# Kernel tuning notes

Measured on AMD Instinct MI355X. Metric: run time of the kernel, lower is better.

## Reference

```python
import jax, jax.numpy as jnp
import numpy as np

B, NQ, D, H, L, P, FFN = 32, 300, 256, 8, 3, 4, 1024
SPATIAL = [(80, 80), (40, 40), (20, 20)]  # static multi-scale feature shapes (640px, strides 8/16/32)
S = sum(h * w for h, w in SPATIAL)  # 8400
HD = D // H


def _ln(x, g, b, eps=1e-5):
    m = jnp.mean(x, -1, keepdims=True)
    v = jnp.mean((x - m) ** 2, -1, keepdims=True)
    return (x - m) * jax.lax.rsqrt(v + eps) * g + b


def _grid_sample(img, grid):
    # img: (N,C,Hh,Ww); grid: (N,Q,Pp,2) in [-1,1]; bilinear, zeros padding, align_corners=False
    N, C, Hh, Ww = img.shape
    x = (grid[..., 0] + 1.0) * (Ww * 0.5) - 0.5
    y = (grid[..., 1] + 1.0) * (Hh * 0.5) - 0.5
    x0 = jnp.floor(x)
    y0 = jnp.floor(y)
    wx1 = x - x0
    wy1 = y - y0
    x0i = x0.astype(jnp.int32)
    y0i = y0.astype(jnp.int32)
    flat = img.reshape(N, C, Hh * Ww)
    Q, Pp = grid.shape[1], grid.shape[2]

    def corner(xi, yi, w):
        valid = (xi >= 0) & (xi < Ww) & (yi >= 0) & (yi < Hh)
        idx = jnp.clip(yi, 0, Hh - 1) * Ww + jnp.clip(xi, 0, Ww - 1)
        v = jnp.take_along_axis(flat, idx.reshape(N, 1, Q * Pp), axis=2).reshape(N, C, Q, Pp)
        return v * (w * valid)[:, None]

    return (corner(x0i, y0i, (1 - wx1) * (1 - wy1))
            + corner(x0i + 1, y0i, wx1 * (1 - wy1))
            + corner(x0i, y0i + 1, (1 - wx1) * wy1)
            + corner(x0i + 1, y0i + 1, wx1 * wy1))


def setup_inputs() -> dict:
    key = jax.random.key(0)
    ks = iter(jax.random.split(key, 32))
    inp = {
        'hidden_states': jax.random.normal(next(ks), (B, NQ, D), jnp.float32),
        'position_embeddings': jax.random.normal(next(ks), (B, NQ, D), jnp.float32),
        'reference_points': jax.random.uniform(next(ks), (B, NQ, 1, 4), jnp.float32, 0.1, 0.9),
        'encoder_hidden_states': jax.random.normal(next(ks), (B, S, D), jnp.float32),
    }
    for name, shape in [('Wq', (D, D)), ('Wk', (D, D)), ('Wv', (D, D)), ('Wo', (D, D)),
                        ('Woff', (D, H * L * P * 2)), ('Waw', (D, H * L * P)),
                        ('Wval', (D, D)), ('Wout', (D, D)), ('W1', (D, FFN)), ('W2', (FFN, D))]:
        inp[name] = jax.random.normal(next(ks), shape, jnp.float32) * 0.02
    for name, dim in [('bq', D), ('bk', D), ('bv', D), ('bo', D), ('boff', H * L * P * 2),
                      ('baw', H * L * P), ('bval', D), ('bout', D), ('b1', FFN), ('b2', D)]:
        inp[name] = jnp.zeros((dim,), jnp.float32)
    for g, bname in [('ln1_g', 'ln1_b'), ('ln2_g', 'ln2_b'), ('ln3_g', 'ln3_b')]:
        inp[g] = jnp.ones((D,), jnp.float32)
        inp[bname] = jnp.zeros((D,), jnp.float32)
    return inp


def reference(hidden_states, position_embeddings, reference_points, encoder_hidden_states,
              Wq, bq, Wk, bk, Wv, bv, Wo, bo, ln1_g, ln1_b,
              Woff, boff, Waw, baw, Wval, bval, Wout, bout, ln2_g, ln2_b,
              W1, b1, W2, b2, ln3_g, ln3_b):
    hs = hidden_states
    # ---- self attention (pos-embedded q/k, raw v) ----
    hp = hs + position_embeddings
    q = ((hp @ Wq + bq) * (HD ** -0.5)).reshape(B, NQ, H, HD)
    k = (hp @ Wk + bk).reshape(B, NQ, H, HD)
    v = (hs @ Wv + bv).reshape(B, NQ, H, HD)
    attn = jax.nn.softmax(jnp.einsum('bqhd,bkhd->bhqk', q, k), axis=-1)
    sa = jnp.einsum('bhqk,bkhd->bqhd', attn, v).reshape(B, NQ, D) @ Wo + bo
    hs = _ln(hs + sa, ln1_g, ln1_b)
    # ---- multi-scale deformable cross attention ----
    hp = hs + position_embeddings
    value = (encoder_hidden_states @ Wval + bval).reshape(B, S, H, HD)
    off = (hp @ Woff + boff).reshape(B, NQ, H, L, P, 2)
    aw = jax.nn.softmax((hp @ Waw + baw).reshape(B, NQ, H, L * P), axis=-1).reshape(B, NQ, H, L, P)
    ref = reference_points  # (B,NQ,1,4) boxes -> 4-coord branch
    loc = ref[:, :, None, :, None, :2] + off / P * ref[:, :, None, :, None, 2:] * 0.5
    grids = (2.0 * loc - 1.0).transpose(0, 2, 1, 3, 4, 5).reshape(B * H, NQ, L, P, 2)
    start = 0
    samples = []
    for lvl, (hh, ww) in enumerate(SPATIAL):
        v_l = value[:, start:start + hh * ww]  # (B,hw,H,HD)
        start += hh * ww
        v_l = v_l.transpose(0, 2, 3, 1).reshape(B * H, HD, hh, ww)
        samples.append(_grid_sample(v_l, grids[:, :, lvl]))  # (B*H,HD,NQ,P)
    sampled = jnp.stack(samples, axis=3).reshape(B * H, HD, NQ, L * P)
    w = aw.transpose(0, 2, 1, 3, 4).reshape(B * H, 1, NQ, L * P)
    ca = (sampled * w).sum(-1).reshape(B, H * HD, NQ).transpose(0, 2, 1) @ Wout + bout
    hs = _ln(hs + ca, ln2_g, ln2_b)
    # ---- FFN ----
    ff = jax.nn.relu(hs @ W1 + b1) @ W2 + b2
    return _ln(hs + ff, ln3_g, ln3_b)
```

## Files before the change

kernel.cpp:

```cpp
#include <hip/hip_runtime.h>
#include <hip/hip_bf16.h>

typedef unsigned int  uint32;
typedef unsigned short ushort16;
typedef __bf16 bfx8 __attribute__((ext_vector_type(8)));
typedef float  f32x4 __attribute__((ext_vector_type(4)));

typedef __attribute__((address_space(1))) const unsigned int gas_u32;
typedef __attribute__((address_space(3))) unsigned int las_u32;

#define B_   32
#define NQ_  300
#define D_   256
#define H_   8
#define HD_  32
#define L_   3
#define P_   4
#define S_   8400
#define FFN_ 1024
#define M1   (B_*NQ_)
#define MV   (B_*S_)
#define NQP  320
#define NQT  19

__device__ inline ushort16 f2bf(float x) {
  uint32 u = __float_as_uint(x);
  uint32 r = u + 0x7fffu + ((u >> 16) & 1u);
  return (ushort16)(r >> 16);
}
__device__ inline uint32 cvtpk(float lo, float hi) {
  uint32 r; asm("v_cvt_pk_bf16_f32 %0, %1, %2" : "=v"(r) : "v"(lo), "v"(hi)); return r;
}

struct WPrep {
  const float* src[9];
  ushort16*    dst[9];
  int K[9], N[9], Npad[9], tileEnd[9];
  float scale[9];
  const float* wval; ushort16* wvalc;
  const float* bqs;  const float* bks;  float* bqk;
  const float* boffs; const float* baws; float* boffaw;
};

__global__ __launch_bounds__(256) void rt_wprep(WPrep a)
{
  __shared__ float t[32][33];
  int blk = blockIdx.x;
  if (blk < 904) {
    int wi = 0;
    while (blk >= a.tileEnd[wi]) wi++;
    int base = wi ? a.tileEnd[wi - 1] : 0;
    int idx = blk - base;
    int K = a.K[wi], N = a.N[wi];
    int ntx = a.Npad[wi] / 32;
    int n0 = (idx % ntx) * 32, k0 = (idx / ntx) * 32;
    float sc = a.scale[wi];
    const float* W = a.src[wi];
    ushort16* WT = a.dst[wi];
    int c = threadIdx.x & 31, r = threadIdx.x >> 5;
#pragma unroll
    for (int i = 0; i < 4; i++) {
      int nn = n0 + c;
      t[r + i * 8][c] = (nn < N) ? W[(size_t)(k0 + r + i * 8) * N + nn] : 0.f;
    }
    __syncthreads();
#pragma unroll
    for (int i = 0; i < 4; i++)
      WT[(size_t)(n0 + r + i * 8) * K + k0 + c] = f2bf(t[c][r + i * 8] * sc);
  } else if (blk < 936) {
    int gid = (blk - 904) * 256 + threadIdx.x;
    int c = gid >> 8, n = gid & 255;
    const float* W = a.wval;
    uint4 u;
    u.x = (uint32)f2bf(W[(c*8+0)*256 + n]) | ((uint32)f2bf(W[(c*8+1)*256 + n]) << 16);
    u.y = (uint32)f2bf(W[(c*8+2)*256 + n]) | ((uint32)f2bf(W[(c*8+3)*256 + n]) << 16);
    u.z = (uint32)f2bf(W[(c*8+4)*256 + n]) | ((uint32)f2bf(W[(c*8+5)*256 + n]) << 16);
    u.w = (uint32)f2bf(W[(c*8+6)*256 + n]) | ((uint32)f2bf(W[(c*8+7)*256 + n]) << 16);
    *(uint4*)&a.wvalc[(size_t)c * 2048 + n * 8] = u;
  } else if (blk == 936) {
    a.bqk[threadIdx.x] = a.bqs[threadIdx.x] * a.scale[0];
  } else if (blk == 937) {
    a.bqk[256 + threadIdx.x] = a.bks[threadIdx.x];
  } else if (blk == 938) {
    if (threadIdx.x < 192) a.boffaw[threadIdx.x] = a.boffs[threadIdx.x];
  } else {
    if (threadIdx.x < 96) a.boffaw[192 + threadIdx.x] = a.baws[threadIdx.x];
  }
}

__global__ __launch_bounds__(1024, 1) void rt_vgemm(
    const float* __restrict__ A, const ushort16* __restrict__ BC,
    const float* __restrict__ bias, ushort16* __restrict__ Vout)
{
  __shared__ __align__(16) char ldsB[131072];
  const int tid = threadIdx.x;
  const int lane = tid & 63, w = tid >> 6;
  const int l15 = lane & 15, l4 = lane >> 4;

#pragma unroll
  for (int i = 0; i < 8; ++i)
    __builtin_amdgcn_global_load_lds(
        (gas_u32*)(const void*)((const char*)BC + tid * 16 + i * 16384),
        (las_u32*)(void*)(&ldsB[tid * 16 + i * 16384]), 16, 0, 0);
  __syncthreads();

  const int wrow = w * 16 + l15;
  for (int t = blockIdx.x; t < MV / 256; t += 256) {
    const float* Ap = A + ((size_t)t * 256 + wrow) * 256 + l4 * 8;
    f32x4 aA = *(const f32x4*)(Ap);
    f32x4 aB = *(const f32x4*)(Ap + 4);
    f32x4 aC = *(const f32x4*)(Ap + 32);
    f32x4 aD = *(const f32x4*)(Ap + 36);
    f32x4 acc[16];
#pragma unroll
    for (int i = 0; i < 16; ++i) acc[i] = (f32x4){0.f, 0.f, 0.f, 0.f};

#pragma unroll
    for (int tt = 0; tt < 4; ++tt) {
      {
        uint4 u;
        u.x = cvtpk(aA[0], aA[1]); u.y = cvtpk(aA[2], aA[3]);
        u.z = cvtpk(aB[0], aB[1]); u.w = cvtpk(aB[2], aB[3]);
        bfx8 af = __builtin_bit_cast(bfx8, u);
        if (tt < 3) {
          aA = *(const f32x4*)(Ap + (2 * tt + 2) * 32);
          aB = *(const f32x4*)(Ap + (2 * tt + 2) * 32 + 4);
        }
        const char* bp = &ldsB[(2 * tt * 4 + l4) * 4096 + l15 * 16];
#pragma unroll
        for (int ni = 0; ni < 16; ++ni) {
          bfx8 bg = *(const bfx8*)(const void*)(bp + ni * 256);
          acc[ni] = __builtin_amdgcn_mfma_f32_16x16x32_bf16(bg, af, acc[ni], 0, 0, 0);
        }
      }
      {
        uint4 u;
        u.x = cvtpk(aC[0], aC[1]); u.y = cvtpk(aC[2], aC[3]);
        u.z = cvtpk(aD[0], aD[1]); u.w = cvtpk(aD[2], aD[3]);
        bfx8 af = __builtin_bit_cast(bfx8, u);
        if (tt < 3) {
          aC = *(const f32x4*)(Ap + (2 * tt + 3) * 32);
          aD = *(const f32x4*)(Ap + (2 * tt + 3) * 32 + 4);
        }
        const char* bp = &ldsB[((2 * tt + 1) * 4 + l4) * 4096 + l15 * 16];
#pragma unroll
        for (int ni = 0; ni < 16; ++ni) {
          bfx8 bg = *(const bfx8*)(const void*)(bp + ni * 256);
          acc[ni] = __builtin_amdgcn_mfma_f32_16x16x32_bf16(bg, af, acc[ni], 0, 0, 0);
        }
      }
    }
    int row = t * 256 + wrow;
    int bb = row / S_, s = row - bb * S_;
    ushort16* vb = Vout + (((size_t)bb * H_) * S_ + s) * HD_;
#pragma unroll
    for (int ni = 0; ni < 16; ++ni) {
      int col = ni * 16 + l4 * 4;
      f32x4 bv = *(const f32x4*)(bias + col);
      int hh = col >> 5, hd = col & 31;
      uint2 st;
      st.x = cvtpk(acc[ni][0] + bv[0], acc[ni][1] + bv[1]);
      st.y = cvtpk(acc[ni][2] + bv[2], acc[ni][3] + bv[3]);
      *(uint2*)(vb + (size_t)hh * S_ * HD_ + hd) = st;
    }
  }
}

#define GBM 128
#define GBN 128
#define GBK 32
#define LDP 40

__global__ __launch_bounds__(256) void rt_mgemm(
    const float* __restrict__ A, const float* __restrict__ A2,
    const ushort16* __restrict__ BT, const float* __restrict__ bias,
    float* __restrict__ C,
    ushort16* __restrict__ Sc, ushort16* __restrict__ Sc2,
    int M, int N, int K, float scale, int mode)
{
  __shared__ __align__(16) ushort16 As[GBM][LDP];
  __shared__ __align__(16) ushort16 Bs[GBN][LDP];
  const int tid  = threadIdx.x;
  const int lane = tid & 63;
  const int w    = tid >> 6;
  const int wr   = (w >> 1) * 64;
  const int wc   = (w & 1) * 64;
  const int bm   = blockIdx.y * GBM;
  const int bn   = blockIdx.x * GBN;
  const int l15  = lane & 15;
  const int l4   = lane >> 4;

  f32x4 acc[4][4];
#pragma unroll
  for (int i = 0; i < 4; i++)
#pragma unroll
    for (int j = 0; j < 4; j++)
      acc[i][j] = (f32x4){0.f, 0.f, 0.f, 0.f};

  const int arow = tid >> 3, akc = tid & 7;
  const int brow = tid >> 2, bkc = tid & 3;

  for (int k0 = 0; k0 < K; k0 += GBK) {
#pragma unroll
    for (int i = 0; i < 4; i++) {
      int row = arow + i * 32;
      f32x4 v = *(const f32x4*)(A + (size_t)(bm + row) * K + k0 + akc * 4);
      if (A2) {
        f32x4 v2 = *(const f32x4*)(A2 + (size_t)(bm + row) * K + k0 + akc * 4);
#pragma unroll
        for (int r = 0; r < 4; r++) v[r] += v2[r];
      }
      uint2 u;
      u.x = cvtpk(v.x, v.y);
      u.y = cvtpk(v.z, v.w);
      *(uint2*)(&As[row][akc * 4]) = u;
    }
#pragma unroll
    for (int i = 0; i < 2; i++) {
      int row = brow + i * 64;
      uint4 v = *(const uint4*)(BT + (size_t)(bn + row) * K + k0 + bkc * 8);
      *(uint4*)(&Bs[row][bkc * 8]) = v;
    }
    __syncthreads();

    bfx8 af[4], bg[4];
#pragma unroll
    for (int mi = 0; mi < 4; mi++)
      af[mi] = *(const bfx8*)(&As[wr + mi * 16 + l15][l4 * 8]);
#pragma unroll
    for (int ni = 0; ni < 4; ni++)
      bg[ni] = *(const bfx8*)(&Bs[wc + ni * 16 + l15][l4 * 8]);
#pragma unroll
    for (int mi = 0; mi < 4; mi++)
#pragma unroll
      for (int ni = 0; ni < 4; ni++)
        acc[mi][ni] = __builtin_amdgcn_mfma_f32_16x16x32_bf16(af[mi], bg[ni], acc[mi][ni], 0, 0, 0);
    __syncthreads();
  }

#pragma unroll
  for (int mi = 0; mi < 4; mi++) {
#pragma unroll
    for (int ni = 0; ni < 4; ni++) {
      int col = bn + wc + ni * 16 + l15;
      if (col >= N) continue;
      float bv = bias[col];
#pragma unroll
      for (int r = 0; r < 4; r++) {
        int row = bm + wr + mi * 16 + l4 * 4 + r;
        float vv = (acc[mi][ni][r] + bv) * scale;
        if (mode == 1) vv = fmaxf(vv, 0.f);
        if (mode == 3) {
          int bb = row / NQ_, q = row - bb * NQ_;
          int hh = col >> 5, hd = col & 31;
          Sc[(((size_t)bb * H_ + hh) * NQP + q) * HD_ + hd] = f2bf(vv);
        } else if (mode == 4) {
          int bb = row / NQ_, q = row - bb * NQ_;
          int hh = col >> 5, hd = col & 31;
          ushort16* d = (hh < 8) ? Sc : Sc2;
          d[(((size_t)bb * H_ + (hh & 7)) * NQP + q) * HD_ + hd] = f2bf(vv);
        } else {
          C[(size_t)row * N + col] = vv;
        }
      }
    }
  }
}

__global__ __launch_bounds__(256) void rt_vtr(const ushort16* __restrict__ vh,
                                              ushort16* __restrict__ vt)
{
  __shared__ ushort16 t[64][33];
  int bh = blockIdx.x;
  const ushort16* src = vh + (size_t)bh * NQP * HD_;
  ushort16* dst = vt + (size_t)bh * HD_ * NQP;
  int tid = threadIdx.x;
  int lrow = tid >> 2, lc8 = (tid & 3) * 8;
  int ohd = tid >> 3, oq8 = (tid & 7) * 8;
  for (int r0 = 0; r0 < NQP; r0 += 64) {
    uint4 v = {0u, 0u, 0u, 0u};
    if (r0 + lrow < NQ_)
      v = *(const uint4*)(src + (size_t)(r0 + lrow) * HD_ + lc8);
    ushort16* tp = &t[lrow][lc8];
    tp[0] = (ushort16)(v.x & 0xffff); tp[1] = (ushort16)(v.x >> 16);
    tp[2] = (ushort16)(v.y & 0xffff); tp[3] = (ushort16)(v.y >> 16);
    tp[4] = (ushort16)(v.z & 0xffff); tp[5] = (ushort16)(v.z >> 16);
    tp[6] = (ushort16)(v.w & 0xffff); tp[7] = (ushort16)(v.w >> 16);
    __syncthreads();
    uint4 o;
    o.x = (uint32)t[oq8 + 0][ohd] | ((uint32)t[oq8 + 1][ohd] << 16);
    o.y = (uint32)t[oq8 + 2][ohd] | ((uint32)t[oq8 + 3][ohd] << 16);
    o.z = (uint32)t[oq8 + 4][ohd] | ((uint32)t[oq8 + 5][ohd] << 16);
    o.w = (uint32)t[oq8 + 6][ohd] | ((uint32)t[oq8 + 7][ohd] << 16);
    *(uint4*)(dst + (size_t)ohd * NQP + r0 + oq8) = o;
    __syncthreads();
  }
}

__global__ __launch_bounds__(256) void rt_fattn(
    const ushort16* __restrict__ qh, const ushort16* __restrict__ kh,
    const ushort16* __restrict__ vt, float* __restrict__ O)
{
  int gw  = blockIdx.x * 4 + (threadIdx.x >> 6);
  int bh  = gw / NQT, qt = gw - bh * NQT;
  int b   = bh >> 3, h = bh & 7;
  int lane = threadIdx.x & 63;
  int l15 = lane & 15, l4 = lane >> 4;
  int kb4 = l4 * 4;
  const ushort16* Qb = qh + (size_t)bh * NQP * HD_;
  const ushort16* Kb = kh + (size_t)bh * NQP * HD_;
  const ushort16* Vb = vt + (size_t)bh * HD_ * NQP;
  int q = qt * 16 + l15;

  bfx8 bgQ = *(const bfx8*)(const void*)(Qb + (size_t)q * HD_ + l4 * 8);
  f32x4 o0 = {0.f,0.f,0.f,0.f}, o1 = {0.f,0.f,0.f,0.f};
  float m = -1e30f, ssum = 0.f;

  for (int k0 = 0; k0 < NQP; k0 += 32) {
    bfx8 afk0 = *(const bfx8*)(const void*)(Kb + (size_t)(k0 + l15) * HD_ + l4 * 8);
    bfx8 afk1 = *(const bfx8*)(const void*)(Kb + (size_t)(k0 + 16 + l15) * HD_ + l4 * 8);
    f32x4 z = {0.f,0.f,0.f,0.f};
    f32x4 s0 = __builtin_amdgcn_mfma_f32_16x16x32_bf16(afk0, bgQ, z, 0, 0, 0);
    f32x4 s1 = __builtin_amdgcn_mfma_f32_16x16x32_bf16(afk1, bgQ, z, 0, 0, 0);
    int ka = k0 + kb4, kbb = k0 + 16 + kb4;
#pragma unroll
    for (int r = 0; r < 4; r++) {
      if (ka  + r >= NQ_) s0[r] = -1e30f;
      if (kbb + r >= NQ_) s1[r] = -1e30f;
    }
    float cm = fmaxf(fmaxf(fmaxf(s0[0], s0[1]), fmaxf(s0[2], s0[3])),
                     fmaxf(fmaxf(s1[0], s1[1]), fmaxf(s1[2], s1[3])));
    cm = fmaxf(cm, __shfl_xor(cm, 16));
    cm = fmaxf(cm, __shfl_xor(cm, 32));
    float nm = fmaxf(m, cm);
    float sc = __expf(m - nm);
    m = nm;
    f32x4 p0, p1;
#pragma unroll
    for (int r = 0; r < 4; r++) { p0[r] = __expf(s0[r] - m); p1[r] = __expf(s1[r] - m); }
    float ls = (p0[0]+p0[1]+p0[2]+p0[3]) + (p1[0]+p1[1]+p1[2]+p1[3]);
    ls += __shfl_xor(ls, 16);
    ls += __shfl_xor(ls, 32);
    ssum = ssum * sc + ls;

    uint32 t0w0 = cvtpk(p0[0], p0[1]);
    uint32 t0w1 = cvtpk(p0[2], p0[3]);
    uint32 t1w0 = cvtpk(p1[0], p1[1]);
    uint32 t1w1 = cvtpk(p1[2], p1[3]);
    int srcA = l15 + 32 * (l4 & 1);
    int srcB = srcA + 16;
    uint32 a00 = __shfl((int)t0w0, srcA), a01 = __shfl((int)t0w1, srcA);
    uint32 b00 = __shfl((int)t0w0, srcB), b01 = __shfl((int)t0w1, srcB);
    uint32 a10 = __shfl((int)t1w0, srcA), a11 = __shfl((int)t1w1, srcA);
    uint32 b10 = __shfl((int)t1w0, srcB), b11 = __shfl((int)t1w1, srcB);
    bool hi = (l4 >= 2);
    uint4 pw;
    pw.x = hi ? a10 : a00;
    pw.y = hi ? a11 : a01;
    pw.z = hi ? b10 : b00;
    pw.w = hi ? b11 : b01;
    bfx8 bgP = __builtin_bit_cast(bfx8, pw);

    bfx8 afv0 = *(const bfx8*)(const void*)(Vb + (size_t)l15 * NQP + k0 + l4 * 8);
    bfx8 afv1 = *(const bfx8*)(const void*)(Vb + (size_t)(16 + l15) * NQP + k0 + l4 * 8);
#pragma unroll
    for (int r = 0; r < 4; r++) { o0[r] *= sc; o1[r] *= sc; }
    o0 = __builtin_amdgcn_mfma_f32_16x16x32_bf16(afv0, bgP, o0, 0, 0, 0);
    o1 = __builtin_amdgcn_mfma_f32_16x16x32_bf16(afv1, bgP, o1, 0, 0, 0);
  }

  if (q < NQ_) {
    float inv = 1.f / ssum;
    float* op = O + ((size_t)(b * NQ_ + q)) * D_ + h * HD_ + kb4;
    f32x4 r0, r1;
#pragma unroll
    for (int r = 0; r < 4; r++) { r0[r] = o0[r] * inv; r1[r] = o1[r] * inv; }
    *(f32x4*)op = r0;
    *(f32x4*)(op + 16) = r1;
  }
}

__global__ __launch_bounds__(256) void rt_ln2(
    const float* __restrict__ X, const float* __restrict__ R1,
    const float* __restrict__ R2,
    const float* __restrict__ g, const float* __restrict__ be,
    float* __restrict__ O, int rows)
{
  int row = blockIdx.x * 4 + (threadIdx.x >> 6);
  int lane = threadIdx.x & 63;
  if (row >= rows) return;
  size_t base = (size_t)row * D_ + lane * 4;
  float4 x = *(const float4*)(X + base);
  float4 r = *(const float4*)(R1 + base);
  float v0 = x.x + r.x, v1 = x.y + r.y, v2 = x.z + r.z, v3 = x.w + r.w;
  if (R2) {
    float4 r2 = *(const float4*)(R2 + base);
    v0 += r2.x; v1 += r2.y; v2 += r2.z; v3 += r2.w;
  }
  float s = v0 + v1 + v2 + v3;
  float sq = v0*v0 + v1*v1 + v2*v2 + v3*v3;
#pragma unroll
  for (int o = 32; o >= 1; o >>= 1) { s += __shfl_xor(s, o); sq += __shfl_xor(sq, o); }
  float mean = s * (1.f / D_);
  float var  = sq * (1.f / D_) - mean * mean;
  float inv  = 1.f / sqrtf(var + 1e-5f);
  int c = lane * 4;
  float4 gv = *(const float4*)(g + c);
  float4 bv = *(const float4*)(be + c);
  float4 o4;
  o4.x = (v0 - mean) * inv * gv.x + bv.x;
  o4.y = (v1 - mean) * inv * gv.y + bv.y;
  o4.z = (v2 - mean) * inv * gv.z + bv.z;
  o4.w = (v3 - mean) * inv * gv.w + bv.w;
  *(float4*)(O + base) = o4;
}

__device__ inline void rt_acc8(const ushort16* p, float wgt, float* acc) {
  uint4 v = *(const uint4*)(const void*)p;
  acc[0] += wgt * __uint_as_float(v.x << 16);
  acc[1] += wgt * __uint_as_float(v.x & 0xffff0000u);
  acc[2] += wgt * __uint_as_float(v.y << 16);
  acc[3] += wgt * __uint_as_float(v.y & 0xffff0000u);
  acc[4] += wgt * __uint_as_float(v.z << 16);
  acc[5] += wgt * __uint_as_float(v.z & 0xffff0000u);
  acc[6] += wgt * __uint_as_float(v.w << 16);
  acc[7] += wgt * __uint_as_float(v.w & 0xffff0000u);
}

__global__ __launch_bounds__(256) void rt_deform(
    const ushort16* __restrict__ value,
    const float* __restrict__ offaw,
    const float* __restrict__ ref,
    float* __restrict__ O)
{
  int gid = blockIdx.x * 256 + threadIdx.x;
  int hd0 = (gid & 3) * 8;
  int bqh = gid >> 2;
  int h   = bqh & 7;
  int bq  = bqh >> 3;
  int b   = bq / NQ_;
  const float* rp = ref + (size_t)bq * 4;
  float rx = rp[0], ry = rp[1];
  float rw = rp[2] * 0.125f, rh = rp[3] * 0.125f;
  const float* op = offaw + (size_t)bq * 288 + h * 24;
  const float* ap = offaw + (size_t)bq * 288 + 192 + h * 12;
  float e[12]; float mx = -1e30f;
#pragma unroll
  for (int i = 0; i < 12; i++) { e[i] = ap[i]; mx = fmaxf(mx, e[i]); }
  float ssum = 0.f;
#pragma unroll
  for (int i = 0; i < 12; i++) { e[i] = __expf(e[i] - mx); ssum += e[i]; }
  float sinv = 1.f / ssum;

  const ushort16* vb = value + ((size_t)b * H_ + h) * (size_t)S_ * HD_ + hd0;
  float acc[8];
#pragma unroll
  for (int i = 0; i < 8; i++) acc[i] = 0.f;
  const int starts[3] = {0, 6400, 8000};
  const int dims[3]   = {80, 40, 20};
#pragma unroll
  for (int l = 0; l < L_; l++) {
    const int Wl = dims[l];
    const ushort16* vl = vb + (size_t)starts[l] * HD_;
#pragma unroll
    for (int p = 0; p < P_; p++) {
      int ip = l * P_ + p;
      float wgt = e[ip] * sinv;
      float x = (rx + op[ip*2+0] * rw) * Wl - 0.5f;
      float y = (ry + op[ip*2+1] * rh) * Wl - 0.5f;
      float x0f = floorf(x), y0f = floorf(y);
      int   x0 = (int)x0f,  y0 = (int)y0f;
      float wx1 = x - x0f, wy1 = y - y0f;
      float wx0 = 1.f - wx1, wy0 = 1.f - wy1;
      bool xok0 = (x0 >= 0) & (x0 < Wl), xok1 = (x0+1 >= 0) & (x0+1 < Wl);
      bool yok0 = (y0 >= 0) & (y0 < Wl), yok1 = (y0+1 >= 0) & (y0+1 < Wl);
      const ushort16* r0p = vl + (size_t)(y0 * Wl) * HD_;
      const ushort16* r1p = r0p + (size_t)Wl * HD_;
      if (xok0 & yok0) rt_acc8(r0p + (size_t)x0 * HD_,     wgt * wx0 * wy0, acc);
      if (xok1 & yok0) rt_acc8(r0p + (size_t)(x0+1) * HD_, wgt * wx1 * wy0, acc);
      if (xok0 & yok1) rt_acc8(r1p + (size_t)x0 * HD_,     wgt * wx0 * wy1, acc);
      if (xok1 & yok1) rt_acc8(r1p + (size_t)(x0+1) * HD_, wgt * wx1 * wy1, acc);
    }
  }
  float* outp = O + (size_t)bq * D_ + h * HD_ + hd0;
  float4 a0, a1;
  a0.x = acc[0]; a0.y = acc[1]; a0.z = acc[2]; a0.w = acc[3];
  a1.x = acc[4]; a1.y = acc[5]; a1.z = acc[6]; a1.w = acc[7];
  *(float4*)outp = a0;
  *(float4*)(outp + 4) = a1;
}

extern "C" void kernel_launch(void* const* d_in, const int* in_sizes, int n_in,
                              void* d_out, int out_size, void* d_ws, size_t ws_size,
                              hipStream_t stream)
{
  const float* hs   = (const float*)d_in[0];
  const float* pos  = (const float*)d_in[1];
  const float* ref  = (const float*)d_in[2];
  const float* ehs  = (const float*)d_in[3];
  const float* Wq   = (const float*)d_in[4];
  const float* Wk   = (const float*)d_in[5];
  const float* Wv   = (const float*)d_in[6];
  const float* Wo   = (const float*)d_in[7];
  const float* Woff = (const float*)d_in[8];
  const float* Waw  = (const float*)d_in[9];
  const float* Wval = (const float*)d_in[10];
  const float* Wout = (const float*)d_in[11];
  const float* W1   = (const float*)d_in[12];
  const float* W2   = (const float*)d_in[13];
  const float* bq   = (const float*)d_in[14];
  const float* bk   = (const float*)d_in[15];
  const float* bvv  = (const float*)d_in[16];
  const float* bo   = (const float*)d_in[17];
  const float* boff = (const float*)d_in[18];
  const float* baw  = (const float*)d_in[19];
  const float* bval = (const float*)d_in[20];
  const float* bout = (const float*)d_in[21];
  const float* b1   = (const float*)d_in[22];
  const float* b2   = (const float*)d_in[23];
  const float* ln1g = (const float*)d_in[24];
  const float* ln1b = (const float*)d_in[25];
  const float* ln2g = (const float*)d_in[26];
  const float* ln2b = (const float*)d_in[27];
  const float* ln3g = (const float*)d_in[28];
  const float* ln3b = (const float*)d_in[29];
  float* out = (float*)d_out;

  float* ws = (float*)d_ws;
  ushort16* value = (ushort16*)ws;
  float* t0     = ws + 36864000;
  float* t1     = ws + 39321600;
  float* hs1    = ws + 41779200;
  float* hs2    = ws + 44236800;
  float* offawb = ws + 46694400;
  float* ffn1   = ws + 49459200;
  ushort16* qh = (ushort16*)(ws + 59289600);
  ushort16* kh = (ushort16*)(ws + 60600320);
  ushort16* vh = (ushort16*)(ws + 61911040);
  ushort16* vt = (ushort16*)(ws + 63221760);
  ushort16* wbase  = (ushort16*)(ws + 64532480);
  ushort16* WqkT   = wbase;
  ushort16* WvT    = WqkT   + 131072;
  ushort16* WoT    = WvT    + 65536;
  ushort16* WoffawT= WoT    + 65536;
  ushort16* WoutT  = WoffawT+ 98304;
  ushort16* W1T    = WoutT  + 65536;
  ushort16* W2T    = W1T    + 262144;
  ushort16* WvalC  = W2T    + 262144;
  float* bqk    = (float*)(WvalC + 65536);
  float* boffaw = bqk + 512;

  const float qscale = 0.17677669529663687f;

  WPrep a;
  a.src[0]=Wq;   a.dst[0]=WqkT;            a.K[0]=256;  a.N[0]=256;  a.Npad[0]=256; a.scale[0]=qscale;
  a.src[1]=Wk;   a.dst[1]=WqkT+65536;      a.K[1]=256;  a.N[1]=256;  a.Npad[1]=256; a.scale[1]=1.f;
  a.src[2]=Wv;   a.dst[2]=WvT;             a.K[2]=256;  a.N[2]=256;  a.Npad[2]=256; a.scale[2]=1.f;
  a.src[3]=Wo;   a.dst[3]=WoT;             a.K[3]=256;  a.N[3]=256;  a.Npad[3]=256; a.scale[3]=1.f;
  a.src[4]=Woff; a.dst[4]=WoffawT;         a.K[4]=256;  a.N[4]=192;  a.Npad[4]=192; a.scale[4]=1.f;
  a.src[5]=Waw;  a.dst[5]=WoffawT+49152;   a.K[5]=256;  a.N[5]=96;   a.Npad[5]=96;  a.scale[5]=1.f;
  a.src[6]=Wout; a.dst[6]=WoutT;           a.K[6]=256;  a.N[6]=256;  a.Npad[6]=256; a.scale[6]=1.f;
  a.src[7]=W1;   a.dst[7]=W1T;             a.K[7]=256;  a.N[7]=1024; a.Npad[7]=1024;a.scale[7]=1.f;
  a.src[8]=W2;   a.dst[8]=W2T;             a.K[8]=1024; a.N[8]=256;  a.Npad[8]=256; a.scale[8]=1.f;
  int cum = 0;
  int tiles[9] = {64, 64, 64, 64, 48, 24, 64, 256, 256};
  for (int i = 0; i < 9; i++) { cum += tiles[i]; a.tileEnd[i] = cum; }
  a.wval = Wval; a.wvalc = WvalC;
  a.bqs = bq; a.bks = bk; a.bqk = bqk;
  a.boffs = boff; a.baws = baw; a.boffaw = boffaw;
  rt_wprep<<<dim3(940), 256, 0, stream>>>(a);

  rt_vgemm<<<dim3(256), 1024, 0, stream>>>(ehs, WvalC, bval, value);

  rt_mgemm<<<dim3(4, M1/GBM), 256, 0, stream>>>(hs, pos, WqkT, bqk, nullptr, qh, kh, M1, 512, 256, 1.f, 4);
  rt_mgemm<<<dim3(2, M1/GBM), 256, 0, stream>>>(hs, nullptr, WvT, bvv, nullptr, vh, nullptr, M1, 256, 256, 1.f, 3);
  rt_vtr<<<dim3(B_*H_), 256, 0, stream>>>(vh, vt);
  rt_fattn<<<dim3(B_*H_*NQT/4), 256, 0, stream>>>(qh, kh, vt, t0);
  rt_mgemm<<<dim3(2, M1/GBM), 256, 0, stream>>>(t0, nullptr, WoT, bo, t1, nullptr, nullptr, M1, 256, 256, 1.f, 0);
  rt_ln2<<<dim3(M1/4), 256, 0, stream>>>(hs, t1, nullptr, ln1g, ln1b, hs1, M1);
  rt_mgemm<<<dim3(3, M1/GBM), 256, 0, stream>>>(hs1, pos, WoffawT, boffaw, offawb, nullptr, nullptr, M1, 288, 256, 1.f, 0);
  rt_deform<<<dim3(M1*H_*4/256), 256, 0, stream>>>(value, offawb, ref, t0);
  rt_mgemm<<<dim3(2, M1/GBM), 256, 0, stream>>>(t0, nullptr, WoutT, bout, t1, nullptr, nullptr, M1, 256, 256, 1.f, 0);
  rt_ln2<<<dim3(M1/4), 256, 0, stream>>>(hs1, t1, nullptr, ln2g, ln2b, hs2, M1);
  rt_mgemm<<<dim3(8, M1/GBM), 256, 0, stream>>>(hs2, nullptr, W1T, b1, ffn1, nullptr, nullptr, M1, FFN_, 256, 1.f, 1);
  rt_mgemm<<<dim3(2, M1/GBM), 256, 0, stream>>>(ffn1, nullptr, W2T, b2, t1, nullptr, nullptr, M1, 256, 1024, 1.f, 0);
  rt_ln2<<<dim3(M1/4), 256, 0, stream>>>(hs2, t1, nullptr, ln3g, ln3b, out, M1);
}
```

Before: 412.2 us.

## Split value-projection GEMM across column halves to double blocks and halve LDS

The value projection kernel now splits the 256 output columns into two 128-column halves, each handled by a separate block, so the grid doubles to 512 blocks. Each block loads only half of the bf16 weight into a 64 KB LDS buffer and keeps 8 accumulators instead of 16. The launch bound no longer forces one block per CU. The aim is more resident waves per CU and fewer registers per thread, to hide latency on the large 268800x256 input stream. The cost is that each fp32 A row is now read from global memory twice, once per column half, and converted to bf16 twice.

```diff
diff --git a/kernel.cpp b/kernel.cpp
--- a/kernel.cpp
+++ b/kernel.cpp
@@ -88,74 +88,64 @@
   }
 }
 
-__global__ __launch_bounds__(1024, 1) void rt_vgemm(
+__global__ __launch_bounds__(1024) void rt_vgemm(
     const float* __restrict__ A, const ushort16* __restrict__ BC,
     const float* __restrict__ bias, ushort16* __restrict__ Vout)
 {
-  __shared__ __align__(16) char ldsB[131072];
+  __shared__ __align__(16) char ldsB[65536];
   const int tid = threadIdx.x;
   const int lane = tid & 63, w = tid >> 6;
   const int l15 = lane & 15, l4 = lane >> 4;
-
-#pragma unroll
-  for (int i = 0; i < 8; ++i)
+  const int cid = blockIdx.x >> 8;
+  const int rg  = blockIdx.x & 255;
+
+#pragma unroll
+  for (int i = 0; i < 4; ++i) {
+    int g = tid * 16 + i * 16384;
+    int kc = g >> 11;
     __builtin_amdgcn_global_load_lds(
-        (gas_u32*)(const void*)((const char*)BC + tid * 16 + i * 16384),
-        (las_u32*)(void*)(&ldsB[tid * 16 + i * 16384]), 16, 0, 0);
+        (gas_u32*)(const void*)((const char*)BC + g + (kc + cid) * 2048),
+        (las_u32*)(void*)(&ldsB[g]), 16, 0, 0);
+  }
   __syncthreads();
 
   const int wrow = w * 16 + l15;
-  for (int t = blockIdx.x; t < MV / 256; t += 256) {
-    const float* Ap = A + ((size_t)t * 256 + wrow) * 256 + l4 * 8;
-    f32x4 aA = *(const f32x4*)(Ap);
-    f32x4 aB = *(const f32x4*)(Ap + 4);
-    f32x4 aC = *(const f32x4*)(Ap + 32);
-    f32x4 aD = *(const f32x4*)(Ap + 36);
-    f32x4 acc[16];
-#pragma unroll
-    for (int i = 0; i < 16; ++i) acc[i] = (f32x4){0.f, 0.f, 0.f, 0.f};
-
-#pragma unroll
-    for (int tt = 0; tt < 4; ++tt) {
-      {
-        uint4 u;
-        u.x = cvtpk(aA[0], aA[1]); u.y = cvtpk(aA[2], aA[3]);
-        u.z = cvtpk(aB[0], aB[1]); u.w = cvtpk(aB[2], aB[3]);
-        bfx8 af = __builtin_bit_cast(bfx8, u);
-        if (tt < 3) {
-          aA = *(const f32x4*)(Ap + (2 * tt + 2) * 32);
-          aB = *(const f32x4*)(Ap + (2 * tt + 2) * 32 + 4);
-        }
-        const char* bp = &ldsB[(2 * tt * 4 + l4) * 4096 + l15 * 16];
-#pragma unroll
-        for (int ni = 0; ni < 16; ++ni) {
-          bfx8 bg = *(const bfx8*)(const void*)(bp + ni * 256);
-          acc[ni] = __builtin_amdgcn_mfma_f32_16x16x32_bf16(bg, af, acc[ni], 0, 0, 0);
-        }
+  const float* Abase = A + (size_t)wrow * 256 + l4 * 8;
+
+  for (int t = rg; t < MV / 256; t += 256) {
+    const float* Ap = Abase + (size_t)t * 65536;
+    f32x4 acc[8];
+#pragma unroll
+    for (int i = 0; i < 8; ++i) acc[i] = (f32x4){0.f, 0.f, 0.f, 0.f};
+
+    f32x4 c0 = *(const f32x4*)(Ap);
+    f32x4 c1 = *(const f32x4*)(Ap + 4);
+#pragma unroll
+    for (int ts = 0; ts < 8; ++ts) {
+      f32x4 n0, n1;
+      if (ts < 7) {
+        n0 = *(const f32x4*)(Ap + (ts + 1) * 32);
+        n1 = *(const f32x4*)(Ap + (ts + 1) * 32 + 4);
       }
-      {
-        uint4 u;
-        u.x = cvtpk(aC[0], aC[1]); u.y = cvtpk(aC[2], aC[3]);
-        u.z = cvtpk(aD[0], aD[1]); u.w = cvtpk(aD[2], aD[3]);
-        bfx8 af = __builtin_bit_cast(bfx8, u);
-        if (tt < 3) {
-          aC = *(const f32x4*)(Ap + (2 * tt + 3) * 32);
-          aD = *(const f32x4*)(Ap + (2 * tt + 3) * 32 + 4);
-        }
-        const char* bp = &ldsB[((2 * tt + 1) * 4 + l4) * 4096 + l15 * 16];
-#pragma unroll
-        for (int ni = 0; ni < 16; ++ni) {
-          bfx8 bg = *(const bfx8*)(const void*)(bp + ni * 256);
-          acc[ni] = __builtin_amdgcn_mfma_f32_16x16x32_bf16(bg, af, acc[ni], 0, 0, 0);
-        }
+      uint4 u;
+      u.x = cvtpk(c0[0], c0[1]); u.y = cvtpk(c0[2], c0[3]);
+      u.z = cvtpk(c1[0], c1[1]); u.w = cvtpk(c1[2], c1[3]);
+      bfx8 af = __builtin_bit_cast(bfx8, u);
+      const char* bp = &ldsB[(ts * 4 + l4) * 2048 + l15 * 16];
+#pragma unroll
+      for (int ni = 0; ni < 8; ++ni) {
+        bfx8 bg = *(const bfx8*)(const void*)(bp + ni * 256);
+        acc[ni] = __builtin_amdgcn_mfma_f32_16x16x32_bf16(bg, af, acc[ni], 0, 0, 0);
       }
-    }
+      c0 = n0; c1 = n1;
+    }
+
     int row = t * 256 + wrow;
     int bb = row / S_, s = row - bb * S_;
     ushort16* vb = Vout + (((size_t)bb * H_) * S_ + s) * HD_;
 #pragma unroll
-    for (int ni = 0; ni < 16; ++ni) {
-      int col = ni * 16 + l4 * 4;
+    for (int ni = 0; ni < 8; ++ni) {
+      int col = cid * 128 + ni * 16 + l4 * 4;
       f32x4 bv = *(const f32x4*)(bias + col);
       int hh = col >> 5, hd = col & 31;
       uint2 st;
@@ -570,7 +560,7 @@
   a.boffs = boff; a.baws = baw; a.boffaw = boffaw;
   rt_wprep<<<dim3(940), 256, 0, stream>>>(a);
 
-  rt_vgemm<<<dim3(256), 1024, 0, stream>>>(ehs, WvalC, bval, value);
+  rt_vgemm<<<dim3(512), 1024, 0, stream>>>(ehs, WvalC, bval, value);
 
   rt_mgemm<<<dim3(4, M1/GBM), 256, 0, stream>>>(hs, pos, WqkT, bqk, nullptr, qh, kh, M1, 512, 256, 1.f, 4);
   rt_mgemm<<<dim3(2, M1/GBM), 256, 0, stream>>>(hs, nullptr, WvT, bvv, nullptr, vh, nullptr, M1, 256, 256, 1.f, 3);
```

New measurement: 446.0 us. 1.08x slower.
